# Optimization experiments

Hardware: AMD Instinct MI355X
Metric: run time of the kernel (lower is better)

Reference implementation:

```python
import jax, jax.numpy as jnp
import numpy as np
import math

IN_CH = 32
OUT_CH = 32
NODE_NUM = 24
BATCH = 32768
# skeleton edges: self-loops + chain (parent -> child), matching init_kwargs
_SRC = list(range(24)) + list(range(23))
_DST = list(range(24)) + list(range(1, 24))


def _build_mask():
    # block mask: block (dst, src) of size [OUT_CH, IN_CH] set to 1 per edge
    m = np.zeros((OUT_CH * NODE_NUM, IN_CH * NODE_NUM), dtype=np.float32)
    for s, d in zip(_SRC, _DST):
        m[OUT_CH * d:OUT_CH * (d + 1), IN_CH * s:IN_CH * (s + 1)] = 1.0
    return jnp.asarray(m)


def setup_inputs() -> dict:
    key = jax.random.key(0)
    kx, kw, kb = jax.random.split(key, 3)
    mask = _build_mask()
    dim = IN_CH * NODE_NUM
    # kaiming-uniform-like per-block init approximated by scaled normal; only
    # values inside mask blocks matter (forward multiplies by mask anyway)
    weight = jax.random.normal(kw, (OUT_CH * NODE_NUM, dim), dtype=jnp.float32) * (1.0 / math.sqrt(IN_CH))
    bound = 1.0 / math.sqrt(dim)
    bias = jax.random.uniform(kb, (OUT_CH * NODE_NUM,), dtype=jnp.float32, minval=-bound, maxval=bound)
    x = jax.random.normal(kx, (BATCH, dim), dtype=jnp.float32)
    return {"x": x, "weight": weight, "bias": bias, "mask": mask}


def reference(x, weight, bias, mask):
    # F.linear(x, weight * mask, bias) == x @ (weight*mask)^T + bias
    w = weight * mask
    return jnp.einsum("bi,oi->bo", x, w) + bias
```

## Files before the change

### kernel.cpp

```cpp
#include <hip/hip_runtime.h>
#include <hip/hip_bf16.h>


typedef __bf16 bf16x8 __attribute__((ext_vector_type(8)));
typedef float  f32x4  __attribute__((ext_vector_type(4)));

#define DIM 768

__device__ __forceinline__ bf16x8 cvt8(const float* __restrict__ p) {
    float4 lo = *(const float4*)p;
    float4 hi = *(const float4*)(p + 4);
    bf16x8 r;
    r[0] = (__bf16)lo.x; r[1] = (__bf16)lo.y; r[2] = (__bf16)lo.z; r[3] = (__bf16)lo.w;
    r[4] = (__bf16)hi.x; r[5] = (__bf16)hi.y; r[6] = (__bf16)hi.z; r[7] = (__bf16)hi.w;
    return r;
}

__global__ __launch_bounds__(256, 4)
void skeleton_linear_kernel(const float* __restrict__ x,
                            const float* __restrict__ w,
                            const float* __restrict__ bias,
                            float* __restrict__ out)
{
    const int tid  = threadIdx.x;
    const int lane = tid & 63;
    const int wave = tid >> 6;
    const int quad = lane >> 4;
    const int l16  = lane & 15;

    const long row0 = (long)blockIdx.x * 16;
    const float* xrow = x + (row0 + l16) * DIM;

#pragma unroll
    for (int i = 0; i < 6; ++i) {
        const int d  = wave * 6 + i;
        const int kb = 32 * d - 32;

        f32x4 acc0 = {0.f, 0.f, 0.f, 0.f};
        f32x4 acc1 = {0.f, 0.f, 0.f, 0.f};

#pragma unroll
        for (int kt = 0; kt < 2; ++kt) {
            if (d == 0 && kt == 0) continue;
            const int k0 = kb + 32 * kt + 8 * quad;
            bf16x8 a = cvt8(xrow + k0);
            const float* w0 = w + (long)(32 * d + l16) * DIM + k0;
            acc0 = __builtin_amdgcn_mfma_f32_16x16x32_bf16(a, cvt8(w0), acc0, 0, 0, 0);
            acc1 = __builtin_amdgcn_mfma_f32_16x16x32_bf16(a, cvt8(w0 + 16 * DIM), acc1, 0, 0, 0);
        }

        const float bi0 = bias[32 * d + l16];
        const float bi1 = bias[32 * d + 16 + l16];
        float* o = out + (row0 + 4 * quad) * DIM + 32 * d + l16;
#pragma unroll
        for (int r = 0; r < 4; ++r) {
            o[(long)r * DIM]      = acc0[r] + bi0;
            o[(long)r * DIM + 16] = acc1[r] + bi1;
        }
    }
}

extern "C" void kernel_launch(void* const* d_in, const int* in_sizes, int n_in,
                              void* d_out, int out_size, void* d_ws, size_t ws_size,
                              hipStream_t stream) {
    const float* x    = (const float*)d_in[0];
    const float* w    = (const float*)d_in[1];
    const float* bias = (const float*)d_in[2];
    float* out = (float*)d_out;

    const int BATCH = 32768;
    dim3 grid(BATCH / 16);
    skeleton_linear_kernel<<<grid, 256, 0, stream>>>(x, w, bias, out);
}
```

Baseline: 232.4 us.

## Stage x and output tiles through LDS and prepack weight fragments to bf16

A small pre-kernel converts the nonzero weight blocks into bf16 MFMA fragments laid out per lane, so the main kernel no longer loads and converts strided fp32 weight rows. The main kernel now uses 512 threads. Each block loads its 16-row x tile with coalesced float4 reads into padded LDS, and the MFMA operands are read from LDS. Results plus bias are written back to LDS and then stored with coalesced float4 writes. This targets the poorly coalesced global reads and writes of the original. The costs are an extra kernel launch, added barriers, and float4 LDS accesses on an odd 770-float row stride that are not always 16-byte aligned.

```diff
diff --git a/kernel.cpp b/kernel.cpp
--- a/kernel.cpp
+++ b/kernel.cpp
@@ -6,6 +6,8 @@
 typedef float  f32x4  __attribute__((ext_vector_type(4)));
 
 #define DIM 768
+#define STRIDE 770
+#define NFRAG (24 * 2 * 2)
 
 __device__ __forceinline__ bf16x8 cvt8(const float* __restrict__ p) {
     float4 lo = *(const float4*)p;
@@ -16,46 +18,97 @@
     return r;
 }
 
-__global__ __launch_bounds__(256, 4)
+__global__ void prepack_w_kernel(const float* __restrict__ w, bf16x8* __restrict__ ws)
+{
+    const int fid = blockIdx.x * 256 + threadIdx.x;
+    const int lane = fid & 63;
+    const int ni   = (fid >> 6) & 1;
+    const int kt   = (fid >> 7) & 1;
+    const int d    = fid >> 8;
+    const int quad = lane >> 4, l16 = lane & 15;
+
+    bf16x8 v;
+    if (d == 0 && kt == 0) {
+#pragma unroll
+        for (int j = 0; j < 8; ++j) v[j] = (__bf16)0.f;
+    } else {
+        const float* src = w + (long)(32 * d + 16 * ni + l16) * DIM
+                             + (32 * d - 32 + 32 * kt + 8 * quad);
+        v = cvt8(src);
+    }
+    ws[fid] = v;
+}
+
+__global__ __launch_bounds__(512, 4)
 void skeleton_linear_kernel(const float* __restrict__ x,
-                            const float* __restrict__ w,
                             const float* __restrict__ bias,
+                            const bf16x8* __restrict__ wfrag,
                             float* __restrict__ out)
 {
+    __shared__ float lds[16 * STRIDE];
+
     const int tid  = threadIdx.x;
     const int lane = tid & 63;
     const int wave = tid >> 6;
     const int quad = lane >> 4;
     const int l16  = lane & 15;
+    const long row0 = (long)blockIdx.x * 16;
 
-    const long row0 = (long)blockIdx.x * 16;
-    const float* xrow = x + (row0 + l16) * DIM;
+    {
+        const float4* gx = (const float4*)(x + row0 * DIM);
+        float4 st[6];
+#pragma unroll
+        for (int i = 0; i < 6; ++i) st[i] = gx[tid + 512 * i];
+#pragma unroll
+        for (int i = 0; i < 6; ++i) {
+            int f = tid + 512 * i;
+            int r = f / 192, c4 = f % 192;
+            *(float4*)&lds[r * STRIDE + 4 * c4] = st[i];
+        }
+    }
+    __syncthreads();
+
+    f32x4 acc[3][2];
+#pragma unroll
+    for (int i = 0; i < 3; ++i) {
+        const int d = wave * 3 + i;
+        f32x4 a0 = {0.f, 0.f, 0.f, 0.f};
+        f32x4 a1 = {0.f, 0.f, 0.f, 0.f};
+#pragma unroll
+        for (int kt = 0; kt < 2; ++kt) {
+            int k0 = 32 * d - 32 + 32 * kt + 8 * quad;
+            int kA = k0 < 0 ? 0 : k0;
+            bf16x8 a = cvt8(&lds[l16 * STRIDE + kA]);
+            const int fb = (d * 2 + kt) * 2;
+            a0 = __builtin_amdgcn_mfma_f32_16x16x32_bf16(a, wfrag[fb * 64 + lane], a0, 0, 0, 0);
+            a1 = __builtin_amdgcn_mfma_f32_16x16x32_bf16(a, wfrag[(fb + 1) * 64 + lane], a1, 0, 0, 0);
+        }
+        acc[i][0] = a0;
+        acc[i][1] = a1;
+    }
+    __syncthreads();
 
 #pragma unroll
-    for (int i = 0; i < 6; ++i) {
-        const int d  = wave * 6 + i;
-        const int kb = 32 * d - 32;
+    for (int i = 0; i < 3; ++i) {
+        const int d = wave * 3 + i;
+#pragma unroll
+        for (int ni = 0; ni < 2; ++ni) {
+            const float bi = bias[32 * d + 16 * ni + l16];
+#pragma unroll
+            for (int r = 0; r < 4; ++r)
+                lds[(4 * quad + r) * STRIDE + 32 * d + 16 * ni + l16] = acc[i][ni][r] + bi;
+        }
+    }
+    __syncthreads();
 
-        f32x4 acc0 = {0.f, 0.f, 0.f, 0.f};
-        f32x4 acc1 = {0.f, 0.f, 0.f, 0.f};
-
+    {
+        float* go = out + row0 * DIM;
 #pragma unroll
-        for (int kt = 0; kt < 2; ++kt) {
-            if (d == 0 && kt == 0) continue;
-            const int k0 = kb + 32 * kt + 8 * quad;
-            bf16x8 a = cvt8(xrow + k0);
-            const float* w0 = w + (long)(32 * d + l16) * DIM + k0;
-            acc0 = __builtin_amdgcn_mfma_f32_16x16x32_bf16(a, cvt8(w0), acc0, 0, 0, 0);
-            acc1 = __builtin_amdgcn_mfma_f32_16x16x32_bf16(a, cvt8(w0 + 16 * DIM), acc1, 0, 0, 0);
-        }
-
-        const float bi0 = bias[32 * d + l16];
-        const float bi1 = bias[32 * d + 16 + l16];
-        float* o = out + (row0 + 4 * quad) * DIM + 32 * d + l16;
-#pragma unroll
-        for (int r = 0; r < 4; ++r) {
-            o[(long)r * DIM]      = acc0[r] + bi0;
-            o[(long)r * DIM + 16] = acc1[r] + bi1;
+        for (int i = 0; i < 6; ++i) {
+            int f = tid + 512 * i;
+            int r = f / 192, c4 = f % 192;
+            float4 v = *(const float4*)&lds[r * STRIDE + 4 * c4];
+            *(float4*)(go + (long)r * DIM + 4 * c4) = v;
         }
     }
 }
@@ -68,7 +121,11 @@
     const float* bias = (const float*)d_in[2];
     float* out = (float*)d_out;
 
+    bf16x8* wpack = (bf16x8*)d_ws;
+
+    prepack_w_kernel<<<NFRAG * 64 / 256, 256, 0, stream>>>(w, wpack);
+
     const int BATCH = 32768;
     dim3 grid(BATCH / 16);
-    skeleton_linear_kernel<<<grid, 256, 0, stream>>>(x, w, bias, out);
+    skeleton_linear_kernel<<<grid, 512, 0, stream>>>(x, bias, wpack, out);
 }
```

New measurement: 187.7 us. -19.3%, faster.

## Prepack weight fragments to bf16 and stage x/out through LDS for coalescing

Applied to the files above, without the earlier changes.

Adds a small prepack kernel that converts the nonzero weight blocks into bf16 MFMA fragment order in workspace, so the main kernel loads one 16-byte fragment per lane instead of converting fp32 weights every block. The main kernel stages each wave's x tiles into padded LDS as bf16 using coalesced row-contiguous loads and reuses the shared 32-column chunk between adjacent nodes. Outputs go through an LDS transpose so global stores become full float4 row writes. This adds a second launch and LDS traffic per tile in exchange for fewer redundant global reads and better coalescing.

```diff
diff --git a/kernel.cpp b/kernel.cpp
--- a/kernel.cpp
+++ b/kernel.cpp
@@ -2,10 +2,14 @@
 #include <hip/hip_bf16.h>
 
 
+typedef __bf16 bf16x4 __attribute__((ext_vector_type(4)));
 typedef __bf16 bf16x8 __attribute__((ext_vector_type(8)));
 typedef float  f32x4  __attribute__((ext_vector_type(4)));
 
 #define DIM 768
+#define XPAD 40
+#define XSLOT (16 * XPAD)
+#define OPAD 36
 
 __device__ __forceinline__ bf16x8 cvt8(const float* __restrict__ p) {
     float4 lo = *(const float4*)p;
@@ -16,47 +20,99 @@
     return r;
 }
 
+__global__ void prepack_w_kernel(const float* __restrict__ w, bf16x8* __restrict__ ws)
+{
+    const int fid = blockIdx.x * 256 + threadIdx.x;
+    const int lane = fid & 63;
+    const int ni   = (fid >> 6) & 1;
+    const int kt   = (fid >> 7) & 1;
+    const int d    = fid >> 8;
+    const int quad = lane >> 4, l16 = lane & 15;
+
+    bf16x8 v;
+    if (d == 0 && kt == 0) {
+#pragma unroll
+        for (int j = 0; j < 8; ++j) v[j] = (__bf16)0.f;
+    } else {
+        const float* src = w + (long)(32 * d + 16 * ni + l16) * DIM
+                             + (32 * d - 32 + 32 * kt + 8 * quad);
+        v = cvt8(src);
+    }
+    ws[fid] = v;
+}
+
 __global__ __launch_bounds__(256, 4)
 void skeleton_linear_kernel(const float* __restrict__ x,
-                            const float* __restrict__ w,
                             const float* __restrict__ bias,
+                            const bf16x8* __restrict__ wfrag,
                             float* __restrict__ out)
 {
+    __shared__ __align__(16) __bf16 xs[4][4 * XSLOT];
+    __shared__ __align__(16) float  os[4][16 * OPAD];
+
     const int tid  = threadIdx.x;
     const int lane = tid & 63;
     const int wave = tid >> 6;
     const int quad = lane >> 4;
     const int l16  = lane & 15;
+    const int d0   = wave * 6;
+    const long row0 = (long)blockIdx.x * 16;
 
-    const long row0 = (long)blockIdx.x * 16;
-    const float* xrow = x + (row0 + l16) * DIM;
+    __bf16* __restrict__ xw = xs[wave];
+    float*  __restrict__ ow = os[wave];
+
+    const int srow = lane >> 3;
+    const int sc4  = lane & 7;
+    const float* xbase = x + (row0 + srow) * DIM + 4 * sc4;
+
+    auto stage = [&](int c, int s) {
+        const float* src = xbase + 32 * c;
+        float4 v0 = *(const float4*)src;
+        float4 v1 = *(const float4*)(src + 8 * DIM);
+        bf16x4 b0, b1;
+        b0[0] = (__bf16)v0.x; b0[1] = (__bf16)v0.y; b0[2] = (__bf16)v0.z; b0[3] = (__bf16)v0.w;
+        b1[0] = (__bf16)v1.x; b1[1] = (__bf16)v1.y; b1[2] = (__bf16)v1.z; b1[3] = (__bf16)v1.w;
+        __bf16* dst = xw + s * XSLOT + srow * XPAD + 4 * sc4;
+        *(bf16x4*)dst = b0;
+        *(bf16x4*)(dst + 8 * XPAD) = b1;
+    };
+
+    stage(d0 > 0 ? d0 - 1 : 0, 0);
+    stage(d0, 1);
+    stage(d0 + 1, 2);
 
 #pragma unroll
     for (int i = 0; i < 6; ++i) {
-        const int d  = wave * 6 + i;
-        const int kb = 32 * d - 32;
+        const int d = d0 + i;
+        if (i < 4) stage(d0 + i + 2, (i + 3) & 3);
 
-        f32x4 acc0 = {0.f, 0.f, 0.f, 0.f};
-        f32x4 acc1 = {0.f, 0.f, 0.f, 0.f};
+        const int fb = 4 * d;
+        f32x4 a0 = {0.f, 0.f, 0.f, 0.f};
+        f32x4 a1 = {0.f, 0.f, 0.f, 0.f};
 
-#pragma unroll
-        for (int kt = 0; kt < 2; ++kt) {
-            if (d == 0 && kt == 0) continue;
-            const int k0 = kb + 32 * kt + 8 * quad;
-            bf16x8 a = cvt8(xrow + k0);
-            const float* w0 = w + (long)(32 * d + l16) * DIM + k0;
-            acc0 = __builtin_amdgcn_mfma_f32_16x16x32_bf16(a, cvt8(w0), acc0, 0, 0, 0);
-            acc1 = __builtin_amdgcn_mfma_f32_16x16x32_bf16(a, cvt8(w0 + 16 * DIM), acc1, 0, 0, 0);
+        if (d > 0) {
+            bf16x8 ap = *(const bf16x8*)(xw + (i & 3) * XSLOT + l16 * XPAD + 8 * quad);
+            a0 = __builtin_amdgcn_mfma_f32_16x16x32_bf16(ap, wfrag[(fb + 0) * 64 + lane], a0, 0, 0, 0);
+            a1 = __builtin_amdgcn_mfma_f32_16x16x32_bf16(ap, wfrag[(fb + 1) * 64 + lane], a1, 0, 0, 0);
+        }
+        {
+            bf16x8 as = *(const bf16x8*)(xw + ((i + 1) & 3) * XSLOT + l16 * XPAD + 8 * quad);
+            a0 = __builtin_amdgcn_mfma_f32_16x16x32_bf16(as, wfrag[(fb + 2) * 64 + lane], a0, 0, 0, 0);
+            a1 = __builtin_amdgcn_mfma_f32_16x16x32_bf16(as, wfrag[(fb + 3) * 64 + lane], a1, 0, 0, 0);
         }
 
         const float bi0 = bias[32 * d + l16];
         const float bi1 = bias[32 * d + 16 + l16];
-        float* o = out + (row0 + 4 * quad) * DIM + 32 * d + l16;
 #pragma unroll
         for (int r = 0; r < 4; ++r) {
-            o[(long)r * DIM]      = acc0[r] + bi0;
-            o[(long)r * DIM + 16] = acc1[r] + bi1;
+            ow[(4 * quad + r) * OPAD + l16]      = a0[r] + bi0;
+            ow[(4 * quad + r) * OPAD + 16 + l16] = a1[r] + bi1;
         }
+        float4 o0 = *(const float4*)(ow + srow * OPAD + 4 * sc4);
+        float4 o1 = *(const float4*)(ow + (srow + 8) * OPAD + 4 * sc4);
+        float* gdst = out + (row0 + srow) * DIM + 32 * d + 4 * sc4;
+        *(float4*)gdst = o0;
+        *(float4*)(gdst + 8 * DIM) = o1;
     }
 }
 
@@ -68,7 +124,11 @@
     const float* bias = (const float*)d_in[2];
     float* out = (float*)d_out;
 
+    bf16x8* wpack = (bf16x8*)d_ws;
+
+    prepack_w_kernel<<<24, 256, 0, stream>>>(w, wpack);
+
     const int BATCH = 32768;
     dim3 grid(BATCH / 16);
-    skeleton_linear_kernel<<<grid, 256, 0, stream>>>(x, w, bias, out);
+    skeleton_linear_kernel<<<grid, 256, 0, stream>>>(x, bias, wpack, out);
 }
```

New measurement: 193.2 us. 1.2x faster.
